# Kernel tuning notes

Hardware: AMD Instinct MI355X
Metric: run time of the kernel (lower is better)

The kernel has to match this reference:

```python
import jax, jax.numpy as jnp
import numpy as np

N_HEAD = 12


def setup_inputs() -> dict:
    key = jax.random.key(0)
    k1, k2, k3 = jax.random.split(key, 3)
    B, S, D = 4, 2048, 768
    x = jax.random.normal(k1, (B, S, D), dtype=jnp.float32)
    std = 0.02
    w_attn = jax.random.normal(k2, (D, 3 * D), dtype=jnp.float32) * std
    b_attn = jnp.zeros((3 * D,), dtype=jnp.float32)
    w_proj = jax.random.normal(k3, (D, D), dtype=jnp.float32) * std
    b_proj = jnp.zeros((D,), dtype=jnp.float32)
    return {"x": x, "w_attn": w_attn, "b_attn": b_attn,
            "w_proj": w_proj, "b_proj": b_proj}


def reference(x, w_attn, b_attn, w_proj, b_proj):
    B, S, D = x.shape
    H = N_HEAD
    hd = D // H
    # c_attn: [B,S,3D]
    qkv = jnp.einsum('bsd,de->bse', x, w_attn) + b_attn
    q, k, v = jnp.split(qkv, 3, axis=2)
    # split heads -> [B,H,S,hd]
    q = q.reshape(B, S, H, hd).transpose(0, 2, 1, 3)
    k = k.reshape(B, S, H, hd).transpose(0, 2, 1, 3)
    v = v.reshape(B, S, H, hd).transpose(0, 2, 1, 3)
    # scores [B,H,S,S]; scale=False in original default
    w = jnp.einsum('bhqd,bhkd->bhqk', q, k)
    # original mask trick: w*b + 1e-9*(1-b), b = lower-triangular ones
    mask = jnp.tril(jnp.ones((S, S), dtype=w.dtype))
    w = w * mask + 1e-9 * (1 - mask)
    w = jax.nn.softmax(w, axis=-1)
    a = jnp.einsum('bhqk,bhkd->bhqd', w, v)
    # merge heads -> [B,S,D]
    a = a.transpose(0, 2, 1, 3).reshape(B, S, D)
    # c_proj
    out = jnp.einsum('bsd,de->bse', a, w_proj) + b_proj
    return out
```

## Files before the change

kernel.cpp:

```cpp
#include <hip/hip_runtime.h>
#include <cstdint>

typedef unsigned short u16;
typedef __bf16 bf16;
typedef bf16 bf16x8 __attribute__((ext_vector_type(8)));
typedef u16 u16x4 __attribute__((ext_vector_type(4)));
typedef u16 u16x8 __attribute__((ext_vector_type(8)));
typedef float f32x4 __attribute__((ext_vector_type(4)));

__device__ __forceinline__ u16 f2b(float f) {
    return __builtin_bit_cast(u16, (bf16)f);
}
__device__ __forceinline__ float b2f(u16 u) {
    return __uint_as_float(((unsigned)u) << 16);
}
__device__ __forceinline__ void load_lds16(const void* g, void* l) {
    auto gp = reinterpret_cast<const __attribute__((address_space(1))) void*>(
        reinterpret_cast<uintptr_t>(g));
    auto lp = reinterpret_cast<__attribute__((address_space(3))) void*>(
        reinterpret_cast<uintptr_t>(l));
    __builtin_amdgcn_global_load_lds(gp, lp, 16, 0, 0);
}
__device__ __forceinline__ f32x4 mfma16(bf16x8 a, bf16x8 b, f32x4 c) {
    return __builtin_amdgcn_mfma_f32_16x16x32_bf16(a, b, c, 0, 0, 0);
}

__global__ __launch_bounds__(256) void convx_kernel(const float* __restrict__ x,
                                                    u16* __restrict__ xb, int n4) {
    int i = blockIdx.x * blockDim.x + threadIdx.x;
    int stride = gridDim.x * blockDim.x;
    for (; i < n4; i += stride) {
        float4 v = ((const float4*)x)[i];
        u16x4 r;
        r[0] = f2b(v.x); r[1] = f2b(v.y); r[2] = f2b(v.z); r[3] = f2b(v.w);
        *(u16x4*)&xb[(size_t)i * 4] = r;
    }
}

__global__ __launch_bounds__(256) void wtrans2_kernel(const float* __restrict__ wa,
                                                      const float* __restrict__ wp,
                                                      u16* __restrict__ wTa,
                                                      u16* __restrict__ wTp) {
    __shared__ float tile[32][33];
    const int bx = blockIdx.x;
    const float* w;
    u16* wT;
    int N, n0;
    if (bx < 72) { w = wa; wT = wTa; N = 2304; n0 = bx * 32; }
    else         { w = wp; wT = wTp; N = 768;  n0 = (bx - 72) * 32; }
    const int K = 768;
    int tx = threadIdx.x, ty = threadIdx.y;
    int k0 = blockIdx.y * 32;
#pragma unroll
    for (int i = 0; i < 4; ++i)
        tile[ty + i * 8][tx] = w[(size_t)(k0 + ty + i * 8) * N + n0 + tx];
    __syncthreads();
#pragma unroll
    for (int i = 0; i < 4; ++i)
        wT[(size_t)(n0 + ty + i * 8) * K + k0 + tx] = f2b(tile[tx][ty + i * 8]);
}

template <bool OUT_BF16>
__global__ __launch_bounds__(256, 2) void gemm_kernel(const u16* __restrict__ A,
                                                      const u16* __restrict__ Bt,
                                                      const float* __restrict__ bias,
                                                      void* __restrict__ out,
                                                      int M, int N, int K) {
    __shared__ __align__(16) u16 SMEM[4 * 128 * 64];
    const int tid = threadIdx.x;
    const int wave = tid >> 6, lane = tid & 63;
    const int l15 = lane & 15, lg = lane >> 4;
    const int gx = gridDim.x;
    const int nwg = gx * gridDim.y;
    const int lin = blockIdx.y * gx + blockIdx.x;
    const int swz = (lin & 7) * (nwg >> 3) + (lin >> 3);
    const int tm = (swz / gx) * 128, tn = (swz % gx) * 128;
    const int wr = (wave >> 1) * 64, wc = (wave & 1) * 64;

    f32x4 acc[4][4] = {};

    const int rbase = wave * 8 + (lane >> 3);
    const int sslot = (lane & 7) ^ (rbase & 7);
    const u16* gA = A + (size_t)(tm + rbase) * K + sslot * 8;
    const u16* gB = Bt + (size_t)(tn + rbase) * K + sslot * 8;
    const int woff = wave * 8 * 64;
    const int nkt = K >> 6;

#pragma unroll
    for (int i = 0; i < 4; ++i) {
        load_lds16(gA + (size_t)i * 32 * K, SMEM + woff + i * 32 * 64);
        load_lds16(gB + (size_t)i * 32 * K, SMEM + 8192 + woff + i * 32 * 64);
    }

    for (int kt = 0; kt < nkt; ++kt) {
        __syncthreads();
        const int cur = kt & 1;
        if (kt + 1 < nkt) {
            u16* ldsA = SMEM + (cur ^ 1) * 2 * 8192 + woff;
            u16* ldsB = ldsA + 8192;
#pragma unroll
            for (int i = 0; i < 4; ++i) {
                load_lds16(gA + (size_t)i * 32 * K + (kt + 1) * 64, ldsA + i * 32 * 64);
                load_lds16(gB + (size_t)i * 32 * K + (kt + 1) * 64, ldsB + i * 32 * 64);
            }
        }
        const u16* As = SMEM + cur * 2 * 8192;
        const u16* Bs = As + 8192;
#pragma unroll
        for (int kk = 0; kk < 64; kk += 32) {
            const int sb = kk >> 3;
            bf16x8 af[4], bfr[4];
#pragma unroll
            for (int m = 0; m < 4; ++m) {
                int row = wr + m * 16 + l15;
                af[m] = *(const bf16x8*)&As[row * 64 + (((sb + lg) ^ (row & 7))) * 8];
            }
#pragma unroll
            for (int n = 0; n < 4; ++n) {
                int row = wc + n * 16 + l15;
                bfr[n] = *(const bf16x8*)&Bs[row * 64 + (((sb + lg) ^ (row & 7))) * 8];
            }
#pragma unroll
            for (int m = 0; m < 4; ++m)
#pragma unroll
                for (int n = 0; n < 4; ++n)
                    acc[m][n] = mfma16(bfr[n], af[m], acc[m][n]);
        }
    }

#pragma unroll
    for (int m = 0; m < 4; ++m) {
        const size_t row = (size_t)(tm + wr + m * 16 + l15);
#pragma unroll
        for (int n = 0; n < 4; ++n) {
            const int col = tn + wc + n * 16 + lg * 4;
            f32x4 v = acc[m][n] + *(const f32x4*)&bias[col];
            if constexpr (OUT_BF16) {
                u16x4 pk;
#pragma unroll
                for (int r = 0; r < 4; ++r) pk[r] = f2b(v[r]);
                *(u16x4*)&((u16*)out)[row * N + col] = pk;
            } else {
                *(f32x4*)&((float*)out)[row * N + col] = v;
            }
        }
    }
}

__global__ __launch_bounds__(256) void vtrans_kernel(const u16* __restrict__ qkv,
                                                     u16* __restrict__ vt,
                                                     float* __restrict__ ts_raw) {
    __shared__ __align__(16) u16 tile[64][72];
    __shared__ float red2[64][4];
    const int st = blockIdx.x, bh = blockIdx.y;
    const int b = bh / 12, h = bh % 12;
    const int t = threadIdx.x;
    const int sr = t >> 2, c4 = (t & 3) * 16;
    const u16* src = qkv + (size_t)(b * 2048 + st * 64 + sr) * 2304 + 1536 + h * 64 + c4;
    *(u16x8*)&tile[sr][c4] = *(const u16x8*)src;
    *(u16x8*)&tile[sr][c4 + 8] = *(const u16x8*)(src + 8);
    __syncthreads();
    const int dr = t >> 2, s4 = (t & 3) * 16;
    u16x8 w0, w1;
    float psum = 0.f;
#pragma unroll
    for (int j = 0; j < 8; ++j) {
        w0[j] = tile[s4 + j][dr];
        w1[j] = tile[s4 + 8 + j][dr];
        psum += b2f(w0[j]) + b2f(w1[j]);
    }
    u16* dst = vt + ((size_t)bh * 64 + dr) * 2048 + st * 64 + s4;
    *(u16x8*)dst = w0;
    *(u16x8*)(dst + 8) = w1;
    red2[dr][t & 3] = psum;
    __syncthreads();
    if (t < 64)
        ts_raw[((size_t)bh * 32 + st) * 64 + t] =
            red2[t][0] + red2[t][1] + red2[t][2] + red2[t][3];
}

__global__ __launch_bounds__(256, 5) void attn_kernel(const u16* __restrict__ qkv,
                                                      const u16* __restrict__ vt,
                                                      const float* __restrict__ ts_raw,
                                                      u16* __restrict__ aout) {
    __shared__ __align__(16) u16 Ks[2][64 * 64];
    __shared__ __align__(16) u16 Vs[2][64 * 64];
    const int bh = blockIdx.x;
    const int qt = 31 - blockIdx.y;
    const int b = bh / 12, h = bh % 12;
    const int tid = threadIdx.x, wave = tid >> 6, lane = tid & 63;
    const int l15 = lane & 15, lg = lane >> 4;
    const int q0 = qt * 64 + wave * 16;
    const size_t rowbase = (size_t)b * 2048;

    bf16x8 qf[2];
#pragma unroll
    for (int ks = 0; ks < 2; ++ks)
        qf[ks] = *(const bf16x8*)(qkv + (rowbase + q0 + l15) * 2304 + h * 64 +
                                  ks * 32 + lg * 8);

    f32x4 o[4] = {};
    float mrun = -1e30f;
    float lrun = 0.f;

    const int rbase = wave * 8 + (lane >> 3);
    const int sslot = (lane & 7) ^ (rbase & 7);
    const int sig0 = ((rbase & 0x1C) << 1) | (rbase & 3);
    const u16* gK = qkv + (rowbase + sig0) * 2304 + 768 + h * 64 + sslot * 8;
    const u16* gV = vt + ((size_t)bh * 64 + rbase) * 2048 + sslot * 8;
    const int ldsoff = wave * 8 * 64;

    const int nkt = qt + 1;
#pragma unroll
    for (int i = 0; i < 2; ++i) {
        load_lds16(gK + (size_t)(i * 4) * 2304, &Ks[0][ldsoff + i * 32 * 64]);
        load_lds16(gV + (size_t)(i * 32) * 2048, &Vs[0][ldsoff + i * 32 * 64]);
    }

    for (int kt = 0; kt < nkt; ++kt) {
        __syncthreads();
        const int cur = kt & 1;
        if (kt + 1 < nkt) {
            const int nx = cur ^ 1;
#pragma unroll
            for (int i = 0; i < 2; ++i) {
                load_lds16(gK + (size_t)((kt + 1) * 64 + i * 4) * 2304,
                           &Ks[nx][ldsoff + i * 32 * 64]);
                load_lds16(gV + (size_t)(i * 32) * 2048 + (kt + 1) * 64,
                           &Vs[nx][ldsoff + i * 32 * 64]);
            }
        }

        f32x4 sacc[4] = {};
        __builtin_amdgcn_s_setprio(1);
#pragma unroll
        for (int ks = 0; ks < 2; ++ks) {
#pragma unroll
            for (int n = 0; n < 4; ++n) {
                int row = n * 16 + l15;
                bf16x8 ak = *(const bf16x8*)&Ks[cur][row * 64 +
                                                     (((ks * 4 + lg) ^ (row & 7))) * 8];
                sacc[n] = mfma16(ak, qf[ks], sacc[n]);
            }
        }
        __builtin_amdgcn_s_setprio(0);

        if (kt == qt) {
            const int q = q0 + l15;
            const int kb = kt * 64 + lg * 8;
#pragma unroll
            for (int n = 0; n < 4; ++n) {
                const int kn = kb + (n & 1) * 32 + ((n >> 1) << 2);
#pragma unroll
                for (int r = 0; r < 4; ++r)
                    if (kn + r > q) sacc[n][r] = 1e-9f;
            }
        }

        float mx = fmaxf(fmaxf(sacc[0][0], sacc[0][1]), fmaxf(sacc[0][2], sacc[0][3]));
#pragma unroll
        for (int n = 1; n < 4; ++n)
            mx = fmaxf(mx, fmaxf(fmaxf(sacc[n][0], sacc[n][1]),
                                 fmaxf(sacc[n][2], sacc[n][3])));
        if (__any(mx > mrun + 8.0f)) {
            float rm = fmaxf(mx, __shfl_xor(mx, 16));
            rm = fmaxf(rm, __shfl_xor(rm, 32));
            const float mnew = fmaxf(mrun, rm);
            const float alpha = __expf(mrun - mnew);
            mrun = mnew;
            lrun *= alpha;
#pragma unroll
            for (int dn = 0; dn < 4; ++dn) o[dn] *= alpha;
        }

#pragma unroll
        for (int n = 0; n < 4; ++n)
#pragma unroll
            for (int r = 0; r < 4; ++r) {
                float p = __expf(sacc[n][r] - mrun);
                lrun += p;
                sacc[n][r] = p;
            }
        bf16x8 bp0, bp1;
#pragma unroll
        for (int j = 0; j < 4; ++j) {
            bp0[j]     = (bf16)sacc[0][j];
            bp0[j + 4] = (bf16)sacc[2][j];
            bp1[j]     = (bf16)sacc[1][j];
            bp1[j + 4] = (bf16)sacc[3][j];
        }

        __builtin_amdgcn_s_setprio(1);
#pragma unroll
        for (int ks = 0; ks < 2; ++ks) {
            bf16x8 bp = ks ? bp1 : bp0;
#pragma unroll
            for (int dn = 0; dn < 4; ++dn) {
                int row = dn * 16 + l15;
                bf16x8 av = *(const bf16x8*)&Vs[cur][row * 64 +
                                                     (((ks * 4 + lg) ^ (row & 7))) * 8];
                o[dn] = mfma16(av, bp, o[dn]);
            }
        }
        __builtin_amdgcn_s_setprio(0);
    }

    lrun += __shfl_xor(lrun, 16);
    lrun += __shfl_xor(lrun, 32);

    if (qt < 31) {
        const float nf = (float)((31 - qt) * 64);
        const float mnew = fmaxf(mrun, 1e-9f);
        const float a = __expf(mrun - mnew);
        const float c = __expf(1e-9f - mnew);
        lrun = lrun * a + nf * c;
        f32x4 suf[4] = {};
        for (int t = qt + 1; t < 32; ++t) {
            const float* sp = ts_raw + ((size_t)bh * 32 + t) * 64;
#pragma unroll
            for (int dn = 0; dn < 4; ++dn)
                suf[dn] += *(const f32x4*)&sp[dn * 16 + lg * 4];
        }
#pragma unroll
        for (int dn = 0; dn < 4; ++dn)
            o[dn] = o[dn] * a + suf[dn] * c;
    }

    const float inv = 1.f / lrun;
    const size_t row = rowbase + q0 + l15;
#pragma unroll
    for (int dn = 0; dn < 4; ++dn) {
        u16x4 st;
#pragma unroll
        for (int r = 0; r < 4; ++r) st[r] = f2b(o[dn][r] * inv);
        *(u16x4*)&aout[row * 768 + h * 64 + dn * 16 + lg * 4] = st;
    }
}

extern "C" void kernel_launch(void* const* d_in, const int* in_sizes, int n_in,
                              void* d_out, int out_size, void* d_ws, size_t ws_size,
                              hipStream_t stream) {
    const float* x      = (const float*)d_in[0];
    const float* w_attn = (const float*)d_in[1];
    const float* b_attn = (const float*)d_in[2];
    const float* w_proj = (const float*)d_in[3];
    const float* b_proj = (const float*)d_in[4];
    float* out = (float*)d_out;
    char* ws = (char*)d_ws;

    u16* xb      = (u16*)(ws + 0);
    u16* wTa     = (u16*)(ws + 12582912);
    u16* wTp     = (u16*)(ws + 16121856);
    u16* qkv     = (u16*)(ws + 17301504);
    u16* vt      = (u16*)(ws + 55050240);
    u16* aout    = (u16*)(ws + 67633152);
    float* ts_raw = (float*)(ws + 0);

    convx_kernel<<<dim3(2048), dim3(256), 0, stream>>>(x, xb, 8192 * 768 / 4);
    wtrans2_kernel<<<dim3(96, 24), dim3(32, 8), 0, stream>>>(w_attn, w_proj, wTa, wTp);
    gemm_kernel<true><<<dim3(18, 64), dim3(256), 0, stream>>>(xb, wTa, b_attn,
                                                              (void*)qkv, 8192, 2304, 768);
    vtrans_kernel<<<dim3(32, 48), dim3(256), 0, stream>>>(qkv, vt, ts_raw);
    attn_kernel<<<dim3(48, 32), dim3(256), 0, stream>>>(qkv, vt, ts_raw, aout);
    gemm_kernel<false><<<dim3(6, 64), dim3(256), 0, stream>>>(aout, wTp, b_proj,
                                                              (void*)out, 8192, 768, 768);
}
```

Measured before the change: 210.9 us.

## Fuse prep kernels, fold V transpose into QKV GEMM, use exp2 softmax

Merges the x conversion and the weight transpose into one prep launch. The QKV GEMM epilogue now writes V directly in transposed layout and computes the per-tile column sums, which removes the separate vtrans kernel. Q is pre-scaled by log2(e) in the GEMM epilogue so attention can use exp2 with a scaled mask value and threshold. Attention also keeps a vector row-sum accumulator, unrolls the double-buffered loop by two, and hoists the swizzle offsets. The transposed V stores from the GEMM are strided scalar 2-byte writes, which may be less efficient than the old tiled transpose.

```diff
diff --git a/kernel.cpp b/kernel.cpp
--- a/kernel.cpp
+++ b/kernel.cpp
@@ -14,6 +14,13 @@
 __device__ __forceinline__ float b2f(u16 u) {
     return __uint_as_float(((unsigned)u) << 16);
 }
+__device__ __forceinline__ float ex2(float x) {
+#if __has_builtin(__builtin_amdgcn_exp2f)
+    return __builtin_amdgcn_exp2f(x);
+#else
+    return exp2f(x);
+#endif
+}
 __device__ __forceinline__ void load_lds16(const void* g, void* l) {
     auto gp = reinterpret_cast<const __attribute__((address_space(1))) void*>(
         reinterpret_cast<uintptr_t>(g));
@@ -25,32 +32,36 @@
     return __builtin_amdgcn_mfma_f32_16x16x32_bf16(a, b, c, 0, 0, 0);
 }
 
-__global__ __launch_bounds__(256) void convx_kernel(const float* __restrict__ x,
-                                                    u16* __restrict__ xb, int n4) {
-    int i = blockIdx.x * blockDim.x + threadIdx.x;
-    int stride = gridDim.x * blockDim.x;
-    for (; i < n4; i += stride) {
-        float4 v = ((const float4*)x)[i];
-        u16x4 r;
-        r[0] = f2b(v.x); r[1] = f2b(v.y); r[2] = f2b(v.z); r[3] = f2b(v.w);
-        *(u16x4*)&xb[(size_t)i * 4] = r;
-    }
-}
-
-__global__ __launch_bounds__(256) void wtrans2_kernel(const float* __restrict__ wa,
-                                                      const float* __restrict__ wp,
-                                                      u16* __restrict__ wTa,
-                                                      u16* __restrict__ wTp) {
+#define LOG2E 1.44269504088896340736f
+
+__global__ __launch_bounds__(256) void prep_kernel(const float* __restrict__ x,
+                                                   u16* __restrict__ xb,
+                                                   const float* __restrict__ wa,
+                                                   const float* __restrict__ wp,
+                                                   u16* __restrict__ wTa,
+                                                   u16* __restrict__ wTp) {
     __shared__ float tile[32][33];
     const int bx = blockIdx.x;
+    if (bx < 2048) {
+        const int n4 = 8192 * 768 / 4;
+        int i = bx * 256 + threadIdx.x;
+        for (; i < n4; i += 2048 * 256) {
+            float4 v = ((const float4*)x)[i];
+            u16x4 r;
+            r[0] = f2b(v.x); r[1] = f2b(v.y); r[2] = f2b(v.z); r[3] = f2b(v.w);
+            *(u16x4*)&xb[(size_t)i * 4] = r;
+        }
+        return;
+    }
+    const int idx = bx - 2048;
+    const int nx = idx % 96, ky = idx / 96;
     const float* w;
     u16* wT;
     int N, n0;
-    if (bx < 72) { w = wa; wT = wTa; N = 2304; n0 = bx * 32; }
-    else         { w = wp; wT = wTp; N = 768;  n0 = (bx - 72) * 32; }
-    const int K = 768;
-    int tx = threadIdx.x, ty = threadIdx.y;
-    int k0 = blockIdx.y * 32;
+    if (nx < 72) { w = wa; wT = wTa; N = 2304; n0 = nx * 32; }
+    else         { w = wp; wT = wTp; N = 768;  n0 = (nx - 72) * 32; }
+    const int K = 768, k0 = ky * 32;
+    const int tx = threadIdx.x & 31, ty = threadIdx.x >> 5;
 #pragma unroll
     for (int i = 0; i < 4; ++i)
         tile[ty + i * 8][tx] = w[(size_t)(k0 + ty + i * 8) * N + n0 + tx];
@@ -60,11 +71,13 @@
         wT[(size_t)(n0 + ty + i * 8) * K + k0 + tx] = f2b(tile[tx][ty + i * 8]);
 }
 
-template <bool OUT_BF16>
+template <int MODE>
 __global__ __launch_bounds__(256, 2) void gemm_kernel(const u16* __restrict__ A,
                                                       const u16* __restrict__ Bt,
                                                       const float* __restrict__ bias,
                                                       void* __restrict__ out,
+                                                      u16* __restrict__ vt,
+                                                      float* __restrict__ ts_raw,
                                                       int M, int N, int K) {
     __shared__ __align__(16) u16 SMEM[4 * 128 * 64];
     const int tid = threadIdx.x;
@@ -128,14 +141,54 @@
         }
     }
 
+    if (MODE == 1 && tn >= 1536) {
+        const int b = tm >> 11;
+        const int s0 = (tm & 2047) + wr;
+        const int st = s0 >> 6;
+        const int hh = (tn + wc - 1536) >> 6;
+        const int bh = b * 12 + hh;
+        f32x4 colsum[4] = {};
+#pragma unroll
+        for (int m = 0; m < 4; ++m) {
+            const int s = s0 + m * 16 + l15;
+#pragma unroll
+            for (int n = 0; n < 4; ++n) {
+                const int col = tn + wc + n * 16 + lg * 4;
+                f32x4 v = acc[m][n] + *(const f32x4*)&bias[col];
+                colsum[n] += v;
+                const int dl = n * 16 + lg * 4;
+#pragma unroll
+                for (int r = 0; r < 4; ++r)
+                    vt[((size_t)bh * 64 + dl + r) * 2048 + s] = f2b(v[r]);
+            }
+        }
+#pragma unroll
+        for (int n = 0; n < 4; ++n)
+#pragma unroll
+            for (int off = 1; off < 16; off <<= 1) {
+                colsum[n][0] += __shfl_xor(colsum[n][0], off);
+                colsum[n][1] += __shfl_xor(colsum[n][1], off);
+                colsum[n][2] += __shfl_xor(colsum[n][2], off);
+                colsum[n][3] += __shfl_xor(colsum[n][3], off);
+            }
+        if (l15 == 0) {
+#pragma unroll
+            for (int n = 0; n < 4; ++n)
+                *(f32x4*)&ts_raw[((size_t)bh * 32 + st) * 64 + n * 16 + lg * 4] =
+                    colsum[n];
+        }
+        return;
+    }
+
+    const float sc = (MODE == 1 && tn < 768) ? LOG2E : 1.f;
 #pragma unroll
     for (int m = 0; m < 4; ++m) {
         const size_t row = (size_t)(tm + wr + m * 16 + l15);
 #pragma unroll
         for (int n = 0; n < 4; ++n) {
             const int col = tn + wc + n * 16 + lg * 4;
-            f32x4 v = acc[m][n] + *(const f32x4*)&bias[col];
-            if constexpr (OUT_BF16) {
+            f32x4 v = (acc[m][n] + *(const f32x4*)&bias[col]) * sc;
+            if constexpr (MODE == 1) {
                 u16x4 pk;
 #pragma unroll
                 for (int r = 0; r < 4; ++r) pk[r] = f2b(v[r]);
@@ -145,38 +198,6 @@
             }
         }
     }
-}
-
-__global__ __launch_bounds__(256) void vtrans_kernel(const u16* __restrict__ qkv,
-                                                     u16* __restrict__ vt,
-                                                     float* __restrict__ ts_raw) {
-    __shared__ __align__(16) u16 tile[64][72];
-    __shared__ float red2[64][4];
-    const int st = blockIdx.x, bh = blockIdx.y;
-    const int b = bh / 12, h = bh % 12;
-    const int t = threadIdx.x;
-    const int sr = t >> 2, c4 = (t & 3) * 16;
-    const u16* src = qkv + (size_t)(b * 2048 + st * 64 + sr) * 2304 + 1536 + h * 64 + c4;
-    *(u16x8*)&tile[sr][c4] = *(const u16x8*)src;
-    *(u16x8*)&tile[sr][c4 + 8] = *(const u16x8*)(src + 8);
-    __syncthreads();
-    const int dr = t >> 2, s4 = (t & 3) * 16;
-    u16x8 w0, w1;
-    float psum = 0.f;
-#pragma unroll
-    for (int j = 0; j < 8; ++j) {
-        w0[j] = tile[s4 + j][dr];
-        w1[j] = tile[s4 + 8 + j][dr];
-        psum += b2f(w0[j]) + b2f(w1[j]);
-    }
-    u16* dst = vt + ((size_t)bh * 64 + dr) * 2048 + st * 64 + s4;
-    *(u16x8*)dst = w0;
-    *(u16x8*)(dst + 8) = w1;
-    red2[dr][t & 3] = psum;
-    __syncthreads();
-    if (t < 64)
-        ts_raw[((size_t)bh * 32 + st) * 64 + t] =
-            red2[t][0] + red2[t][1] + red2[t][2] + red2[t][3];
 }
 
 __global__ __launch_bounds__(256, 5) void attn_kernel(const u16* __restrict__ qkv,
@@ -192,6 +213,8 @@
     const int l15 = lane & 15, lg = lane >> 4;
     const int q0 = qt * 64 + wave * 16;
     const size_t rowbase = (size_t)b * 2048;
+    const float MASKVAL = 1e-9f * LOG2E;
+    const float THR2 = 8.0f * LOG2E;
 
     bf16x8 qf[2];
 #pragma unroll
@@ -201,7 +224,7 @@
 
     f32x4 o[4] = {};
     float mrun = -1e30f;
-    float lrun = 0.f;
+    f32x4 lacc = {};
 
     const int rbase = wave * 8 + (lane >> 3);
     const int sslot = (lane & 7) ^ (rbase & 7);
@@ -209,39 +232,27 @@
     const u16* gK = qkv + (rowbase + sig0) * 2304 + 768 + h * 64 + sslot * 8;
     const u16* gV = vt + ((size_t)bh * 64 + rbase) * 2048 + sslot * 8;
     const int ldsoff = wave * 8 * 64;
-
-    const int nkt = qt + 1;
-#pragma unroll
-    for (int i = 0; i < 2; ++i) {
-        load_lds16(gK + (size_t)(i * 4) * 2304, &Ks[0][ldsoff + i * 32 * 64]);
-        load_lds16(gV + (size_t)(i * 32) * 2048, &Vs[0][ldsoff + i * 32 * 64]);
-    }
-
-    for (int kt = 0; kt < nkt; ++kt) {
-        __syncthreads();
-        const int cur = kt & 1;
-        if (kt + 1 < nkt) {
-            const int nx = cur ^ 1;
-#pragma unroll
-            for (int i = 0; i < 2; ++i) {
-                load_lds16(gK + (size_t)((kt + 1) * 64 + i * 4) * 2304,
-                           &Ks[nx][ldsoff + i * 32 * 64]);
-                load_lds16(gV + (size_t)(i * 32) * 2048 + (kt + 1) * 64,
-                           &Vs[nx][ldsoff + i * 32 * 64]);
-            }
-        }
-
+    u16* sK0 = &Ks[0][ldsoff];
+    u16* sK1 = &Ks[1][ldsoff];
+    u16* sV0 = &Vs[0][ldsoff];
+    u16* sV1 = &Vs[1][ldsoff];
+    const int xk0 = ((0 + lg) ^ (l15 & 7)) * 8;
+    const int xk1 = ((4 + lg) ^ (l15 & 7)) * 8;
+
+#define STAGE_PAIR(Kd, Vd, kp, vp)                       \
+    load_lds16(kp, Kd);                                  \
+    load_lds16(kp + (size_t)4 * 2304, Kd + 32 * 64);     \
+    load_lds16(vp, Vd);                                  \
+    load_lds16(vp + (size_t)32 * 2048, Vd + 32 * 64);
+
+    auto process = [&](const u16* Kb, const u16* Vb, int kt) {
         f32x4 sacc[4] = {};
         __builtin_amdgcn_s_setprio(1);
 #pragma unroll
-        for (int ks = 0; ks < 2; ++ks) {
-#pragma unroll
-            for (int n = 0; n < 4; ++n) {
-                int row = n * 16 + l15;
-                bf16x8 ak = *(const bf16x8*)&Ks[cur][row * 64 +
-                                                     (((ks * 4 + lg) ^ (row & 7))) * 8];
-                sacc[n] = mfma16(ak, qf[ks], sacc[n]);
-            }
+        for (int n = 0; n < 4; ++n) {
+            const int ra = (n * 16 + l15) * 64;
+            sacc[n] = mfma16(*(const bf16x8*)&Kb[ra + xk0], qf[0], sacc[n]);
+            sacc[n] = mfma16(*(const bf16x8*)&Kb[ra + xk1], qf[1], sacc[n]);
         }
         __builtin_amdgcn_s_setprio(0);
 
@@ -253,7 +264,7 @@
                 const int kn = kb + (n & 1) * 32 + ((n >> 1) << 2);
 #pragma unroll
                 for (int r = 0; r < 4; ++r)
-                    if (kn + r > q) sacc[n][r] = 1e-9f;
+                    if (kn + r > q) sacc[n][r] = MASKVAL;
             }
         }
 
@@ -262,13 +273,13 @@
         for (int n = 1; n < 4; ++n)
             mx = fmaxf(mx, fmaxf(fmaxf(sacc[n][0], sacc[n][1]),
                                  fmaxf(sacc[n][2], sacc[n][3])));
-        if (__any(mx > mrun + 8.0f)) {
+        if (__any(mx > mrun + THR2)) {
             float rm = fmaxf(mx, __shfl_xor(mx, 16));
             rm = fmaxf(rm, __shfl_xor(rm, 32));
             const float mnew = fmaxf(mrun, rm);
-            const float alpha = __expf(mrun - mnew);
+            const float alpha = ex2(mrun - mnew);
             mrun = mnew;
-            lrun *= alpha;
+            lacc *= alpha;
 #pragma unroll
             for (int dn = 0; dn < 4; ++dn) o[dn] *= alpha;
         }
@@ -276,11 +287,10 @@
 #pragma unroll
         for (int n = 0; n < 4; ++n)
 #pragma unroll
-            for (int r = 0; r < 4; ++r) {
-                float p = __expf(sacc[n][r] - mrun);
-                lrun += p;
-                sacc[n][r] = p;
-            }
+            for (int r = 0; r < 4; ++r)
+                sacc[n][r] = ex2(sacc[n][r] - mrun);
+        lacc += (sacc[0] + sacc[1]) + (sacc[2] + sacc[3]);
+
         bf16x8 bp0, bp1;
 #pragma unroll
         for (int j = 0; j < 4; ++j) {
@@ -292,27 +302,47 @@
 
         __builtin_amdgcn_s_setprio(1);
 #pragma unroll
-        for (int ks = 0; ks < 2; ++ks) {
-            bf16x8 bp = ks ? bp1 : bp0;
-#pragma unroll
-            for (int dn = 0; dn < 4; ++dn) {
-                int row = dn * 16 + l15;
-                bf16x8 av = *(const bf16x8*)&Vs[cur][row * 64 +
-                                                     (((ks * 4 + lg) ^ (row & 7))) * 8];
-                o[dn] = mfma16(av, bp, o[dn]);
-            }
+        for (int dn = 0; dn < 4; ++dn) {
+            const int ra = (dn * 16 + l15) * 64;
+            o[dn] = mfma16(*(const bf16x8*)&Vb[ra + xk0], bp0, o[dn]);
+            o[dn] = mfma16(*(const bf16x8*)&Vb[ra + xk1], bp1, o[dn]);
         }
         __builtin_amdgcn_s_setprio(0);
-    }
-
+    };
+
+    const int nkt = qt + 1;
+    STAGE_PAIR(sK0, sV0, gK, gV);
+    const u16* gKp = gK + (size_t)64 * 2304;
+    const u16* gVp = gV + 64;
+
+    int kt = 0;
+    for (;;) {
+        __syncthreads();
+        if (kt + 1 < nkt) {
+            STAGE_PAIR(sK1, sV1, gKp, gVp);
+            gKp += (size_t)64 * 2304; gVp += 64;
+        }
+        process(Ks[0], Vs[0], kt);
+        if (++kt == nkt) break;
+        __syncthreads();
+        if (kt + 1 < nkt) {
+            STAGE_PAIR(sK0, sV0, gKp, gVp);
+            gKp += (size_t)64 * 2304; gVp += 64;
+        }
+        process(Ks[1], Vs[1], kt);
+        if (++kt == nkt) break;
+    }
+#undef STAGE_PAIR
+
+    float lrun = (lacc[0] + lacc[1]) + (lacc[2] + lacc[3]);
     lrun += __shfl_xor(lrun, 16);
     lrun += __shfl_xor(lrun, 32);
 
     if (qt < 31) {
         const float nf = (float)((31 - qt) * 64);
-        const float mnew = fmaxf(mrun, 1e-9f);
-        const float a = __expf(mrun - mnew);
-        const float c = __expf(1e-9f - mnew);
+        const float mnew = fmaxf(mrun, MASKVAL);
+        const float a = ex2(mrun - mnew);
+        const float c = ex2(MASKVAL - mnew);
         lrun = lrun * a + nf * c;
         f32x4 suf[4] = {};
         for (int t = qt + 1; t < 32; ++t) {
@@ -348,20 +378,21 @@
     float* out = (float*)d_out;
     char* ws = (char*)d_ws;
 
-    u16* xb      = (u16*)(ws + 0);
-    u16* wTa     = (u16*)(ws + 12582912);
-    u16* wTp     = (u16*)(ws + 16121856);
-    u16* qkv     = (u16*)(ws + 17301504);
-    u16* vt      = (u16*)(ws + 55050240);
-    u16* aout    = (u16*)(ws + 67633152);
-    float* ts_raw = (float*)(ws + 0);
-
-    convx_kernel<<<dim3(2048), dim3(256), 0, stream>>>(x, xb, 8192 * 768 / 4);
-    wtrans2_kernel<<<dim3(96, 24), dim3(32, 8), 0, stream>>>(w_attn, w_proj, wTa, wTp);
-    gemm_kernel<true><<<dim3(18, 64), dim3(256), 0, stream>>>(xb, wTa, b_attn,
-                                                              (void*)qkv, 8192, 2304, 768);
-    vtrans_kernel<<<dim3(32, 48), dim3(256), 0, stream>>>(qkv, vt, ts_raw);
+    u16* xb       = (u16*)(ws + 0);
+    u16* wTa      = (u16*)(ws + 12582912);
+    u16* wTp      = (u16*)(ws + 16121856);
+    u16* qkv      = (u16*)(ws + 17301504);
+    u16* vt       = (u16*)(ws + 55050240);
+    float* ts_raw = (float*)(ws + 67633152);
+    u16* aout     = (u16*)(ws + 0);
+
+    prep_kernel<<<dim3(2048 + 2304), dim3(256), 0, stream>>>(x, xb, w_attn, w_proj,
+                                                             wTa, wTp);
+    gemm_kernel<1><<<dim3(18, 64), dim3(256), 0, stream>>>(xb, wTa, b_attn,
+                                                           (void*)qkv, vt, ts_raw,
+                                                           8192, 2304, 768);
     attn_kernel<<<dim3(48, 32), dim3(256), 0, stream>>>(qkv, vt, ts_raw, aout);
-    gemm_kernel<false><<<dim3(6, 64), dim3(256), 0, stream>>>(aout, wTp, b_proj,
-                                                              (void*)out, 8192, 768, 768);
-}
+    gemm_kernel<0><<<dim3(6, 64), dim3(256), 0, stream>>>(aout, wTp, b_proj,
+                                                          (void*)out, nullptr, nullptr,
+                                                          8192, 768, 768);
+}
```

Result: faster. 199.0 us (-5.7%).
